# Performance work log

Hardware: AMD Instinct MI355X
Metric: run time of the kernel (lower is better)

The kernel has to match this reference:

```python
import jax, jax.numpy as jnp
import numpy as np

ITERN = 5  # hard-coded SqrtmLayer(cov_mat, 5)


def setup_inputs() -> dict:
    key = jax.random.key(0)
    k1, k2, k3 = jax.random.split(key, 3)
    B, C, H, W = 16, 64, 256, 256
    R = 8  # reduction
    x = jax.random.normal(k1, (B, C, H, W), dtype=jnp.float32)
    w1 = jax.random.normal(k2, (C // R, C), dtype=jnp.float32) * 0.1
    b1 = jnp.zeros((C // R,), dtype=jnp.float32)
    w2 = jax.random.normal(k3, (C, C // R), dtype=jnp.float32) * 0.1
    b2 = jnp.zeros((C,), dtype=jnp.float32)
    return {"x": x, "w1": w1, "b1": b1, "w2": w2, "b2": b2}


def _covpool(x):
    # x: [B, C, h, w].  y = x @ I_hat @ x^T with I_hat = (1/M)I - (1/M^2)J,
    # which equals centered covariance: (x_c @ x_c^T) / M.
    B, C, h, w = x.shape
    M = h * w
    xf = x.reshape(B, C, M)
    xc = xf - jnp.mean(xf, axis=-1, keepdims=True)
    return jnp.einsum('bcm,bdm->bcd', xc, xc) / M  # [B, C, C]


def _sqrtm_ns(cov, iterN):
    # Newton-Schulz iteration for matrix square root (per-batch [C,C]).
    B, C, _ = cov.shape
    I = jnp.eye(C, dtype=cov.dtype)
    I3 = 3.0 * I
    normA = jnp.einsum('bii->b', cov)  # trace
    A = cov / normA[:, None, None]
    ZY = 0.5 * (I3 - A)
    Y = jnp.matmul(A, ZY)
    Z = ZY
    for _ in range(1, iterN - 1):
        ZY = 0.5 * (I3 - jnp.matmul(Z, Y))
        Y = jnp.matmul(Y, ZY)
        Z = jnp.matmul(ZY, Z)
    ZY = 0.5 * jnp.matmul(Y, I3 - jnp.matmul(Z, Y))
    return ZY * jnp.sqrt(normA)[:, None, None]


def reference(x, w1, b1, w2, b2):
    # h,w < 1000 so the crop branch is identity (x_sub = x)
    cov = _covpool(x)                       # [B, C, C]
    cov_sqrt = _sqrtm_ns(cov, ITERN)        # [B, C, C]
    v = jnp.mean(cov_sqrt, axis=1)          # [B, C] (mean over rows, dim=1)
    hid = jax.nn.relu(jnp.einsum('bc,hc->bh', v, w1) + b1)
    att = jax.nn.sigmoid(jnp.einsum('bh,ch->bc', hid, w2) + b2)
    return att[:, :, None, None] * x
```

## Files before the change

### kernel.cpp

```cpp
#include <hip/hip_runtime.h>
#include <hip/hip_bf16.h>
#include <math.h>

#define BATCH 16
#define CH    64
#define MM    65536
#define PSTRIDE 4160
#define SF    68

typedef __attribute__((ext_vector_type(8))) short s16x8;
typedef __attribute__((ext_vector_type(4))) float f32x4;

__device__ __forceinline__ unsigned short f2bf(float f) {
    __hip_bfloat16 h = __float2bfloat16(f);
    return __builtin_bit_cast(unsigned short, h);
}
__device__ __forceinline__ float bf2f(unsigned short u) {
    return __builtin_bit_cast(float, (unsigned)u << 16);
}

#define UIDX(i, j) ((i) * 4 + (j) - ((i) * ((i) + 1)) / 2)

__global__ __launch_bounds__(256, 3) void gram_mfma(const float* __restrict__ x,
                                                    float* __restrict__ part,
                                                    int nchunk, int chunk_m) {
    int blk = blockIdx.x;
    int b = blk / nchunk, chunk = blk - b * nchunk;
    int t = threadIdx.x, w = t >> 6, l = t & 63;
    int lr = l & 15, lg = l >> 4;
    int mwave = chunk_m >> 2;
    int nck = mwave >> 5;

    const float* xw = x + (size_t)b * CH * MM + (size_t)chunk * chunk_m +
                      (size_t)w * mwave + lg * 8;
    const float* rp0 = xw + (size_t)(lr)      * MM;
    const float* rp1 = xw + (size_t)(16 + lr) * MM;
    const float* rp2 = xw + (size_t)(32 + lr) * MM;
    const float* rp3 = xw + (size_t)(48 + lr) * MM;

    f32x4 acc[10];
    const f32x4 zero = {0.f, 0.f, 0.f, 0.f};
#pragma unroll
    for (int i = 0; i < 10; ++i) acc[i] = zero;
    float ssum0 = 0.f, ssum1 = 0.f, ssum2 = 0.f, ssum3 = 0.f;

    float4 A0, A1, A2, A3, A4, A5, A6, A7;
    float4 B0, B1, B2, B3, B4, B5, B6, B7;

#define LOAD8(P, o) do {                                                      \
        P##0 = *(const float4*)(rp0 + (o));  P##1 = *(const float4*)(rp0 + (o) + 4); \
        P##2 = *(const float4*)(rp1 + (o));  P##3 = *(const float4*)(rp1 + (o) + 4); \
        P##4 = *(const float4*)(rp2 + (o));  P##5 = *(const float4*)(rp2 + (o) + 4); \
        P##6 = *(const float4*)(rp3 + (o));  P##7 = *(const float4*)(rp3 + (o) + 4); \
    } while (0)

#define CVT_ROW(va, vb, fr, ss) do {                                          \
        float e0 = (va).x, e1 = (va).y, e2 = (va).z, e3 = (va).w;             \
        float e4 = (vb).x, e5 = (vb).y, e6 = (vb).z, e7 = (vb).w;             \
        ss += ((e0 + e1) + (e2 + e3)) + ((e4 + e5) + (e6 + e7));              \
        unsigned short* fp = (unsigned short*)&(fr);                          \
        fp[0] = f2bf(e0); fp[1] = f2bf(e1); fp[2] = f2bf(e2); fp[3] = f2bf(e3); \
        fp[4] = f2bf(e4); fp[5] = f2bf(e5); fp[6] = f2bf(e6); fp[7] = f2bf(e7); \
    } while (0)

#define COMPUTE(P) do {                                                       \
        s16x8 fr0, fr1, fr2, fr3;                                             \
        CVT_ROW(P##0, P##1, fr0, ssum0);                                      \
        CVT_ROW(P##2, P##3, fr1, ssum1);                                      \
        CVT_ROW(P##4, P##5, fr2, ssum2);                                      \
        CVT_ROW(P##6, P##7, fr3, ssum3);                                      \
        acc[0] = __builtin_amdgcn_mfma_f32_16x16x32_bf16(fr0, fr0, acc[0], 0, 0, 0); \
        acc[1] = __builtin_amdgcn_mfma_f32_16x16x32_bf16(fr0, fr1, acc[1], 0, 0, 0); \
        acc[2] = __builtin_amdgcn_mfma_f32_16x16x32_bf16(fr0, fr2, acc[2], 0, 0, 0); \
        acc[3] = __builtin_amdgcn_mfma_f32_16x16x32_bf16(fr0, fr3, acc[3], 0, 0, 0); \
        acc[4] = __builtin_amdgcn_mfma_f32_16x16x32_bf16(fr1, fr1, acc[4], 0, 0, 0); \
        acc[5] = __builtin_amdgcn_mfma_f32_16x16x32_bf16(fr1, fr2, acc[5], 0, 0, 0); \
        acc[6] = __builtin_amdgcn_mfma_f32_16x16x32_bf16(fr1, fr3, acc[6], 0, 0, 0); \
        acc[7] = __builtin_amdgcn_mfma_f32_16x16x32_bf16(fr2, fr2, acc[7], 0, 0, 0); \
        acc[8] = __builtin_amdgcn_mfma_f32_16x16x32_bf16(fr2, fr3, acc[8], 0, 0, 0); \
        acc[9] = __builtin_amdgcn_mfma_f32_16x16x32_bf16(fr3, fr3, acc[9], 0, 0, 0); \
    } while (0)

    LOAD8(A, 0);
    for (int c = 0; c < nck; c += 2) {
        LOAD8(B, (c + 1) * 32);
        COMPUTE(A);
        if (c + 2 < nck) LOAD8(A, (c + 2) * 32);
        COMPUTE(B);
    }

    {
        float v;
        v = ssum0; v += __shfl_xor(v, 16); v += __shfl_xor(v, 32); ssum0 = v;
        v = ssum1; v += __shfl_xor(v, 16); v += __shfl_xor(v, 32); ssum1 = v;
        v = ssum2; v += __shfl_xor(v, 16); v += __shfl_xor(v, 32); ssum2 = v;
        v = ssum3; v += __shfl_xor(v, 16); v += __shfl_xor(v, 32); ssum3 = v;
    }

    __shared__ float xs[64 * 65];
    __shared__ float csum[64];
    for (int ww = 0; ww < 4; ++ww) {
        if (w == ww) {
#pragma unroll
            for (int i = 0; i < 4; ++i)
#pragma unroll
                for (int j = 0; j < 4; ++j)
                    if (i <= j) {
#pragma unroll
                        for (int jj = 0; jj < 4; ++jj) {
                            int r = i * 16 + lg * 4 + jj, cc = j * 16 + lr;
                            float v = acc[UIDX(i, j)][jj];
                            if (ww == 0) xs[r * 65 + cc] = v;
                            else         xs[r * 65 + cc] += v;
                        }
                    }
            if (l < 16) {
                if (ww == 0) {
                    csum[l]      = ssum0; csum[16 + l] = ssum1;
                    csum[32 + l] = ssum2; csum[48 + l] = ssum3;
                } else {
                    csum[l]      += ssum0; csum[16 + l] += ssum1;
                    csum[32 + l] += ssum2; csum[48 + l] += ssum3;
                }
            }
        }
        __syncthreads();
    }

    float* op = part + (size_t)blk * PSTRIDE;
#pragma unroll
    for (int rix = 0; rix < 16; ++rix) {
        int e = t + rix * 256;
        int r = e >> 6, cc = e & 63;
        op[e] = ((r >> 4) > (cc >> 4)) ? xs[cc * 65 + r] : xs[r * 65 + cc];
    }
    if (t < 64) op[4096 + t] = csum[t];
}

__global__ __launch_bounds__(256) void reduce_parts(const float* __restrict__ part,
                                                    float* __restrict__ red,
                                                    int nchunk) {
    int b = blockIdx.y;
    int i = blockIdx.x * 256 + threadIdx.x;
    if (i >= PSTRIDE / 4) return;
    const float4* p = reinterpret_cast<const float4*>(part + (size_t)b * nchunk * PSTRIDE) + i;
    float4 s = {0.f, 0.f, 0.f, 0.f};
    for (int ch = 0; ch < nchunk; ++ch) {
        float4 v = p[(size_t)ch * (PSTRIDE / 4)];
        s.x += v.x; s.y += v.y; s.z += v.z; s.w += v.w;
    }
    reinterpret_cast<float4*>(red + (size_t)b * PSTRIDE)[i] = s;
}

__device__ __forceinline__ void cvt_store(const float* __restrict__ M, int row,
                                          int col, unsigned short* Hp,
                                          unsigned short* Lp) {
    float4 v = *reinterpret_cast<const float4*>(M + row * SF + col);
    ushort4 h, lo;
    h.x = f2bf(v.x); lo.x = f2bf(v.x - bf2f(h.x));
    h.y = f2bf(v.y); lo.y = f2bf(v.y - bf2f(h.y));
    h.z = f2bf(v.z); lo.z = f2bf(v.z - bf2f(h.z));
    h.w = f2bf(v.w); lo.w = f2bf(v.w - bf2f(h.w));
    int byte = (row * 128 + col * 2) ^ ((row & 7) << 4);
    *reinterpret_cast<ushort4*>(reinterpret_cast<char*>(Hp) + byte) = h;
    *reinterpret_cast<ushort4*>(reinterpret_cast<char*>(Lp) + byte) = lo;
}

__device__ __forceinline__ void mm64(const float* __restrict__ A,
                                     const float* __restrict__ B,
                                     float* __restrict__ C,
                                     unsigned short* AHp, unsigned short* ALp,
                                     unsigned short* BHp, unsigned short* BLp,
                                     int t) {
    int w = t >> 6, l = t & 63, lg = l >> 4, lr = l & 15;
    __syncthreads();
#pragma unroll
    for (int r = 0; r < 4; ++r) {
        int e4 = t + r * 256;
        int row = e4 >> 4;
        int col = (e4 & 15) << 2;
        cvt_store(A, row, col, AHp, ALp);
        cvt_store(B, row, col, BHp, BLp);
    }
    __syncthreads();
    f32x4 acc[4];
    const f32x4 zero = {0.f, 0.f, 0.f, 0.f};
#pragma unroll
    for (int i = 0; i < 4; ++i) acc[i] = zero;
    int arow = w * 16 + lr;
#pragma unroll
    for (int kk = 0; kk < 2; ++kk) {
        int kbyte = kk * 64 + lg * 16;
        int abyte = (arow * 128 + kbyte) ^ ((arow & 7) << 4);
        s16x8 ah = *reinterpret_cast<const s16x8*>(reinterpret_cast<const char*>(AHp) + abyte);
        s16x8 al = *reinterpret_cast<const s16x8*>(reinterpret_cast<const char*>(ALp) + abyte);
#pragma unroll
        for (int ct = 0; ct < 4; ++ct) {
            int brow = ct * 16 + lr;
            int bbyte = (brow * 128 + kbyte) ^ ((brow & 7) << 4);
            s16x8 bh = *reinterpret_cast<const s16x8*>(reinterpret_cast<const char*>(BHp) + bbyte);
            s16x8 bl = *reinterpret_cast<const s16x8*>(reinterpret_cast<const char*>(BLp) + bbyte);
            acc[ct] = __builtin_amdgcn_mfma_f32_16x16x32_bf16(ah, bh, acc[ct], 0, 0, 0);
            acc[ct] = __builtin_amdgcn_mfma_f32_16x16x32_bf16(ah, bl, acc[ct], 0, 0, 0);
            acc[ct] = __builtin_amdgcn_mfma_f32_16x16x32_bf16(al, bh, acc[ct], 0, 0, 0);
        }
    }
#pragma unroll
    for (int ct = 0; ct < 4; ++ct)
#pragma unroll
        for (int j = 0; j < 4; ++j)
            C[(w * 16 + lg * 4 + j) * SF + ct * 16 + lr] = acc[ct][j];
    __syncthreads();
}

__global__ __launch_bounds__(256) void ns_att(const float* __restrict__ red,
                                              const float* __restrict__ w1,
                                              const float* __restrict__ b1,
                                              const float* __restrict__ w2,
                                              const float* __restrict__ b2,
                                              float* __restrict__ att) {
    __shared__ float BUF[5][64 * SF];
    __shared__ unsigned short AH[64 * 64], AL[64 * 64], BH[64 * 64], BL[64 * 64];
    __shared__ float sv[64];
    __shared__ float hid8[8];
    __shared__ float scal[2];

    int b = blockIdx.x, t = threadIdx.x;
    const float* pb = red + (size_t)b * PSTRIDE;

    if (t < 64) sv[t] = pb[4096 + t];
    __syncthreads();

    const float invM = 1.0f / (float)MM;
    const float invM2 = invM * invM;
#pragma unroll
    for (int r = 0; r < 4; ++r) {
        int e4 = t + r * 256;
        int row = e4 >> 4;
        int col = (e4 & 15) << 2;
        float4 g = *(reinterpret_cast<const float4*>(pb) + e4);
        float sr = sv[row] * invM2;
        BUF[0][row * SF + col]     = g.x * invM - sr * sv[col];
        BUF[0][row * SF + col + 1] = g.y * invM - sr * sv[col + 1];
        BUF[0][row * SF + col + 2] = g.z * invM - sr * sv[col + 2];
        BUF[0][row * SF + col + 3] = g.w * invM - sr * sv[col + 3];
    }
    __syncthreads();

    if (t == 0) {
        float tr = 0.f;
        for (int c = 0; c < 64; ++c) tr += BUF[0][c * SF + c];
        scal[0] = 1.0f / tr;
        scal[1] = sqrtf(tr);
    }
    __syncthreads();
    float itr = scal[0];
#pragma unroll
    for (int rr = 0; rr < 16; ++rr) {
        int e = t + rr * 256;
        BUF[0][(e >> 6) * SF + (e & 63)] *= itr;
    }

    float *pA = BUF[0], *pY = BUF[1], *pZ = BUF[2], *pT = BUF[3], *pS = BUF[4];

    mm64(pA, pA, pT, AH, AL, BH, BL, t);
#pragma unroll
    for (int rr = 0; rr < 16; ++rr) {
        int e = t + rr * 256;
        int r = e >> 6, c = e & 63;
        float a = pA[r * SF + c];
        pY[r * SF + c] = 1.5f * a - 0.5f * pT[r * SF + c];
        pZ[r * SF + c] = (r == c ? 1.5f : 0.f) - 0.5f * a;
    }

    for (int it = 0; it < 3; ++it) {
        mm64(pZ, pY, pT, AH, AL, BH, BL, t);
#pragma unroll
        for (int rr = 0; rr < 16; ++rr) {
            int e = t + rr * 256;
            int r = e >> 6, c = e & 63;
            pT[r * SF + c] = (r == c ? 1.5f : 0.f) - 0.5f * pT[r * SF + c];
        }
        mm64(pY, pT, pS, AH, AL, BH, BL, t);
        mm64(pT, pZ, pA, AH, AL, BH, BL, t);
        float* tmp;
        tmp = pY; pY = pS; pS = tmp;
        tmp = pZ; pZ = pA; pA = tmp;
    }
    mm64(pZ, pY, pT, AH, AL, BH, BL, t);
#pragma unroll
    for (int rr = 0; rr < 16; ++rr) {
        int e = t + rr * 256;
        int r = e >> 6, c = e & 63;
        pT[r * SF + c] = (r == c ? 1.5f : 0.f) - 0.5f * pT[r * SF + c];
    }
    mm64(pY, pT, pS, AH, AL, BH, BL, t);

    if (t < 64) {
        float v = 0.f;
        for (int i = 0; i < 64; ++i) v += pS[t * SF + i];
        sv[t] = v * scal[1] * (1.0f / 64.0f);
    }
    __syncthreads();
    if (t < 8) {
        float h = b1[t];
        for (int c = 0; c < 64; ++c) h += sv[c] * w1[t * 64 + c];
        hid8[t] = h > 0.f ? h : 0.f;
    }
    __syncthreads();
    if (t < 64) {
        float p = b2[t];
        for (int h = 0; h < 8; ++h) p += hid8[h] * w2[t * 8 + h];
        att[b * 64 + t] = 1.0f / (1.0f + expf(-p));
    }
}

__global__ __launch_bounds__(256) void scale_out(const float* __restrict__ x,
                                                 const float* __restrict__ att,
                                                 float* __restrict__ out) {
    size_t i = (size_t)blockIdx.x * blockDim.x + threadIdx.x;
    const size_t total4 = (size_t)BATCH * CH * MM / 4;
    const size_t stride = (size_t)gridDim.x * blockDim.x;
    const float4* x4 = reinterpret_cast<const float4*>(x);
    float4* o4 = reinterpret_cast<float4*>(out);
    for (; i < total4; i += stride) {
        int bc = (int)(i >> 14);
        float a = att[bc];
        float4 v = x4[i];
        v.x *= a; v.y *= a; v.z *= a; v.w *= a;
        o4[i] = v;
    }
}

extern "C" void kernel_launch(void* const* d_in, const int* in_sizes, int n_in,
                              void* d_out, int out_size, void* d_ws, size_t ws_size,
                              hipStream_t stream) {
    const float* x  = (const float*)d_in[0];
    const float* w1 = (const float*)d_in[1];
    const float* b1 = (const float*)d_in[2];
    const float* w2 = (const float*)d_in[3];
    const float* b2 = (const float*)d_in[4];
    float* out = (float*)d_out;
    float* ws  = (float*)d_ws;

    int nchunk = 64;
    for (;;) {
        size_t need = ((size_t)BATCH * nchunk * PSTRIDE + (size_t)BATCH * PSTRIDE +
                       (size_t)BATCH * CH) * sizeof(float);
        if (need <= ws_size || nchunk == 1) break;
        nchunk >>= 1;
    }
    int chunk_m = MM / nchunk;

    float* part = ws;
    float* red  = ws + (size_t)BATCH * nchunk * PSTRIDE;
    float* att  = red + (size_t)BATCH * PSTRIDE;

    gram_mfma<<<BATCH * nchunk, 256, 0, stream>>>(x, part, nchunk, chunk_m);
    reduce_parts<<<dim3((PSTRIDE / 4 + 255) / 256, BATCH), 256, 0, stream>>>(part, red, nchunk);
    ns_att<<<BATCH, 256, 0, stream>>>(red, w1, b1, w2, b2, att);
    scale_out<<<2048, 256, 0, stream>>>(x, att, out);
}
```

Before: 208.5 us.

## Compute row sums via MFMA with ones, use nontemporal stores, widen scale grid

The per-row fp32 sums in the gram kernel become extra bf16 MFMAs against a vector of ones, which removes the scalar add chains and the cross-lane shuffle reduction. Row sums are now taken from bf16-rounded values, which slightly changes the mean correction. Partial-result writes, the reduction reads and the output writes use nontemporal hints to avoid polluting cache. The scale kernel grid is doubled.

Result: faster. 176.3 us (-15.5%).

```diff
diff --git a/kernel.cpp b/kernel.cpp
--- a/kernel.cpp
+++ b/kernel.cpp
@@ -18,8 +18,6 @@
 __device__ __forceinline__ float bf2f(unsigned short u) {
     return __builtin_bit_cast(float, (unsigned)u << 16);
 }
-
-#define UIDX(i, j) ((i) * 4 + (j) - ((i) * ((i) + 1)) / 2)
 
 __global__ __launch_bounds__(256, 3) void gram_mfma(const float* __restrict__ x,
                                                     float* __restrict__ part,
@@ -39,10 +37,19 @@
     const float* rp3 = xw + (size_t)(48 + lr) * MM;
 
     f32x4 acc[10];
+    f32x4 accs[4];
     const f32x4 zero = {0.f, 0.f, 0.f, 0.f};
 #pragma unroll
     for (int i = 0; i < 10; ++i) acc[i] = zero;
-    float ssum0 = 0.f, ssum1 = 0.f, ssum2 = 0.f, ssum3 = 0.f;
+#pragma unroll
+    for (int i = 0; i < 4; ++i) accs[i] = zero;
+
+    s16x8 ones;
+    {
+        unsigned short* op1 = (unsigned short*)&ones;
+#pragma unroll
+        for (int i = 0; i < 8; ++i) op1[i] = 0x3F80;
+    }
 
     float4 A0, A1, A2, A3, A4, A5, A6, A7;
     float4 B0, B1, B2, B3, B4, B5, B6, B7;
@@ -54,21 +61,20 @@
         P##6 = *(const float4*)(rp3 + (o));  P##7 = *(const float4*)(rp3 + (o) + 4); \
     } while (0)
 
-#define CVT_ROW(va, vb, fr, ss) do {                                          \
-        float e0 = (va).x, e1 = (va).y, e2 = (va).z, e3 = (va).w;             \
-        float e4 = (vb).x, e5 = (vb).y, e6 = (vb).z, e7 = (vb).w;             \
-        ss += ((e0 + e1) + (e2 + e3)) + ((e4 + e5) + (e6 + e7));              \
+#define CVT_ROW(va, vb, fr) do {                                              \
         unsigned short* fp = (unsigned short*)&(fr);                          \
-        fp[0] = f2bf(e0); fp[1] = f2bf(e1); fp[2] = f2bf(e2); fp[3] = f2bf(e3); \
-        fp[4] = f2bf(e4); fp[5] = f2bf(e5); fp[6] = f2bf(e6); fp[7] = f2bf(e7); \
+        fp[0] = f2bf((va).x); fp[1] = f2bf((va).y);                           \
+        fp[2] = f2bf((va).z); fp[3] = f2bf((va).w);                           \
+        fp[4] = f2bf((vb).x); fp[5] = f2bf((vb).y);                           \
+        fp[6] = f2bf((vb).z); fp[7] = f2bf((vb).w);                           \
     } while (0)
 
 #define COMPUTE(P) do {                                                       \
         s16x8 fr0, fr1, fr2, fr3;                                             \
-        CVT_ROW(P##0, P##1, fr0, ssum0);                                      \
-        CVT_ROW(P##2, P##3, fr1, ssum1);                                      \
-        CVT_ROW(P##4, P##5, fr2, ssum2);                                      \
-        CVT_ROW(P##6, P##7, fr3, ssum3);                                      \
+        CVT_ROW(P##0, P##1, fr0);                                             \
+        CVT_ROW(P##2, P##3, fr1);                                             \
+        CVT_ROW(P##4, P##5, fr2);                                             \
+        CVT_ROW(P##6, P##7, fr3);                                             \
         acc[0] = __builtin_amdgcn_mfma_f32_16x16x32_bf16(fr0, fr0, acc[0], 0, 0, 0); \
         acc[1] = __builtin_amdgcn_mfma_f32_16x16x32_bf16(fr0, fr1, acc[1], 0, 0, 0); \
         acc[2] = __builtin_amdgcn_mfma_f32_16x16x32_bf16(fr0, fr2, acc[2], 0, 0, 0); \
@@ -79,6 +85,10 @@
         acc[7] = __builtin_amdgcn_mfma_f32_16x16x32_bf16(fr2, fr2, acc[7], 0, 0, 0); \
         acc[8] = __builtin_amdgcn_mfma_f32_16x16x32_bf16(fr2, fr3, acc[8], 0, 0, 0); \
         acc[9] = __builtin_amdgcn_mfma_f32_16x16x32_bf16(fr3, fr3, acc[9], 0, 0, 0); \
+        accs[0] = __builtin_amdgcn_mfma_f32_16x16x32_bf16(ones, fr0, accs[0], 0, 0, 0); \
+        accs[1] = __builtin_amdgcn_mfma_f32_16x16x32_bf16(ones, fr1, accs[1], 0, 0, 0); \
+        accs[2] = __builtin_amdgcn_mfma_f32_16x16x32_bf16(ones, fr2, accs[2], 0, 0, 0); \
+        accs[3] = __builtin_amdgcn_mfma_f32_16x16x32_bf16(ones, fr3, accs[3], 0, 0, 0); \
     } while (0)
 
     LOAD8(A, 0);
@@ -89,13 +99,7 @@
         COMPUTE(B);
     }
 
-    {
-        float v;
-        v = ssum0; v += __shfl_xor(v, 16); v += __shfl_xor(v, 32); ssum0 = v;
-        v = ssum1; v += __shfl_xor(v, 16); v += __shfl_xor(v, 32); ssum1 = v;
-        v = ssum2; v += __shfl_xor(v, 16); v += __shfl_xor(v, 32); ssum2 = v;
-        v = ssum3; v += __shfl_xor(v, 16); v += __shfl_xor(v, 32); ssum3 = v;
-    }
+#define UIDX(i, j) ((i) * 4 + (j) - ((i) * ((i) + 1)) / 2)
 
     __shared__ float xs[64 * 65];
     __shared__ float csum[64];
@@ -116,11 +120,11 @@
                     }
             if (l < 16) {
                 if (ww == 0) {
-                    csum[l]      = ssum0; csum[16 + l] = ssum1;
-                    csum[32 + l] = ssum2; csum[48 + l] = ssum3;
+                    csum[l]      = accs[0][0]; csum[16 + l] = accs[1][0];
+                    csum[32 + l] = accs[2][0]; csum[48 + l] = accs[3][0];
                 } else {
-                    csum[l]      += ssum0; csum[16 + l] += ssum1;
-                    csum[32 + l] += ssum2; csum[48 + l] += ssum3;
+                    csum[l]      += accs[0][0]; csum[16 + l] += accs[1][0];
+                    csum[32 + l] += accs[2][0]; csum[48 + l] += accs[3][0];
                 }
             }
         }
@@ -132,9 +136,10 @@
     for (int rix = 0; rix < 16; ++rix) {
         int e = t + rix * 256;
         int r = e >> 6, cc = e & 63;
-        op[e] = ((r >> 4) > (cc >> 4)) ? xs[cc * 65 + r] : xs[r * 65 + cc];
-    }
-    if (t < 64) op[4096 + t] = csum[t];
+        float v = ((r >> 4) > (cc >> 4)) ? xs[cc * 65 + r] : xs[r * 65 + cc];
+        __builtin_nontemporal_store(v, op + e);
+    }
+    if (t < 64) __builtin_nontemporal_store(csum[t], op + 4096 + t);
 }
 
 __global__ __launch_bounds__(256) void reduce_parts(const float* __restrict__ part,
@@ -143,13 +148,13 @@
     int b = blockIdx.y;
     int i = blockIdx.x * 256 + threadIdx.x;
     if (i >= PSTRIDE / 4) return;
-    const float4* p = reinterpret_cast<const float4*>(part + (size_t)b * nchunk * PSTRIDE) + i;
-    float4 s = {0.f, 0.f, 0.f, 0.f};
+    const f32x4* p = reinterpret_cast<const f32x4*>(part + (size_t)b * nchunk * PSTRIDE) + i;
+    f32x4 s = {0.f, 0.f, 0.f, 0.f};
     for (int ch = 0; ch < nchunk; ++ch) {
-        float4 v = p[(size_t)ch * (PSTRIDE / 4)];
-        s.x += v.x; s.y += v.y; s.z += v.z; s.w += v.w;
-    }
-    reinterpret_cast<float4*>(red + (size_t)b * PSTRIDE)[i] = s;
+        f32x4 v = __builtin_nontemporal_load(p + (size_t)ch * (PSTRIDE / 4));
+        s += v;
+    }
+    reinterpret_cast<f32x4*>(red + (size_t)b * PSTRIDE)[i] = s;
 }
 
 __device__ __forceinline__ void cvt_store(const float* __restrict__ M, int row,
@@ -321,14 +326,14 @@
     size_t i = (size_t)blockIdx.x * blockDim.x + threadIdx.x;
     const size_t total4 = (size_t)BATCH * CH * MM / 4;
     const size_t stride = (size_t)gridDim.x * blockDim.x;
-    const float4* x4 = reinterpret_cast<const float4*>(x);
-    float4* o4 = reinterpret_cast<float4*>(out);
+    const f32x4* x4 = reinterpret_cast<const f32x4*>(x);
+    f32x4* o4 = reinterpret_cast<f32x4*>(out);
     for (; i < total4; i += stride) {
         int bc = (int)(i >> 14);
         float a = att[bc];
-        float4 v = x4[i];
-        v.x *= a; v.y *= a; v.z *= a; v.w *= a;
-        o4[i] = v;
+        f32x4 v = x4[i];
+        v *= a;
+        __builtin_nontemporal_store(v, o4 + i);
     }
 }
 
@@ -359,5 +364,5 @@
     gram_mfma<<<BATCH * nchunk, 256, 0, stream>>>(x, part, nchunk, chunk_m);
     reduce_parts<<<dim3((PSTRIDE / 4 + 255) / 256, BATCH), 256, 0, stream>>>(part, red, nchunk);
     ns_att<<<BATCH, 256, 0, stream>>>(red, w1, b1, w2, b2, att);
-    scale_out<<<2048, 256, 0, stream>>>(x, att, out);
-}
+    scale_out<<<4096, 256, 0, stream>>>(x, att, out);
+}
```
